# Optimization experiments

Hardware: AMD Instinct MI355X
Metric: run time of the kernel (lower is better)

Reference implementation:

```python
import jax, jax.numpy as jnp
import numpy as np

B, H, W, C = 2, 128, 128, 192
HEADS = 6
HD = C // HEADS
WS = 16
OWIN = int(WS * 0.5) + WS          # 24
PAD = (OWIN - WS) // 2             # 4
NQ = WS * WS
NK = OWIN * OWIN
EPS = 1e-6
HID = ((int(C * 2.667) + 7) // 8) * 8  # 512


def _rel_pos_index():
    cq = np.stack(np.meshgrid(np.arange(WS), np.arange(WS), indexing='ij')).reshape(2, -1)
    ck = np.stack(np.meshgrid(np.arange(OWIN), np.arange(OWIN), indexing='ij')).reshape(2, -1)
    rel = (ck[:, None, :] - cq[:, :, None]).transpose(1, 2, 0).astype(np.int64)  # (nq, nk, 2)
    rel[:, :, 0] += WS - 1
    rel[:, :, 1] += WS - 1
    rel[:, :, 0] *= WS + OWIN - 1
    return rel.sum(-1)  # (nq, nk)

RPI = jnp.asarray(_rel_pos_index())


def setup_inputs() -> dict:
    key = jax.random.key(0)
    ks = jax.random.split(key, 16)
    def w(k, shape, s=0.02):
        return jax.random.normal(k, shape, jnp.float32) * s
    return {
        'x': jax.random.normal(ks[0], (B, H * W, C), jnp.float32),
        'qkv_w': w(ks[1], (3 * C, C)), 'qkv_b': jnp.zeros((3 * C,), jnp.float32),
        'proj_w': w(ks[2], (C, C)), 'proj_b': jnp.zeros((C,), jnp.float32),
        'rpb': w(ks[3], ((WS + OWIN - 1) ** 2, HEADS)),
        'n1_w': jnp.ones((C,), jnp.float32), 'n1_b': jnp.zeros((C,), jnp.float32),
        'ls1': jnp.full((C,), 1e-6, jnp.float32),
        'n2_w': jnp.ones((C,), jnp.float32), 'n2_b': jnp.zeros((C,), jnp.float32),
        'ls2': jnp.full((C,), 1e-6, jnp.float32),
        'fcgv_w': w(ks[4], (2 * HID, C)), 'fcgv_b': jnp.zeros((2 * HID,), jnp.float32),
        'dw_w': w(ks[5], (HID, 1, 3, 3)), 'dw_b': jnp.zeros((HID,), jnp.float32),
        'dwd_w': w(ks[6], (HID, 1, 3, 3)), 'dwd_b': jnp.zeros((HID,), jnp.float32),
        'dil_scale': w(ks[7], (1,), 0.1),
        'fco_w': w(ks[8], (C, HID)), 'fco_b': jnp.zeros((C,), jnp.float32),
    }


def _iln(x, wgt, bias):
    # spatially-holistic LN: stats over (L, C); returns normed x and residual scale
    xf = x.astype(jnp.float32)
    mean = xf.mean(axis=(1, 2), keepdims=True)
    var = ((xf - mean) ** 2).mean(axis=(1, 2), keepdims=True)
    std = jnp.sqrt(var + EPS)
    scale = jnp.minimum(std, 2.0)  # std_ema buffer initialized to 1.0 (eval path)
    xn = (xf - mean) / scale
    return (xn * wgt + bias).astype(x.dtype), scale


def _oca(x, qkv_w, qkv_b, proj_w, proj_b, rpb):
    b = x.shape[0]
    nh, nw = H // WS, W // WS
    nwin = b * nh * nw
    qkv = x @ qkv_w.T + qkv_b
    q, k, v = jnp.split(qkv, 3, axis=-1)
    # non-overlapping query windows: (nwin, heads, nq, hd)
    qw = q.reshape(b, nh, WS, nw, WS, C).transpose(0, 1, 3, 2, 4, 5)
    qw = qw.reshape(nwin, NQ, HEADS, HD).transpose(0, 2, 1, 3)
    # overlapping K/V windows via unfold(kernel=OWIN, stride=WS, pad=PAD)
    kv = jnp.concatenate([k, v], axis=-1).reshape(b, H, W, 2 * C).transpose(0, 3, 1, 2)
    kvp = jnp.pad(kv, ((0, 0), (0, 0), (PAD, PAD), (PAD, PAD)))
    ih = (jnp.arange(nh) * WS)[:, None] + jnp.arange(OWIN)[None, :]
    iw = (jnp.arange(nw) * WS)[:, None] + jnp.arange(OWIN)[None, :]
    kvw = kvp[:, :, ih][:, :, :, :, iw]               # (b, 2C, nh, owin, nw, owin)
    kvw = kvw.transpose(0, 2, 4, 3, 5, 1).reshape(nwin, NK, 2 * C)
    kw = kvw[..., :C].reshape(nwin, NK, HEADS, HD).transpose(0, 2, 1, 3)
    vw = kvw[..., C:].reshape(nwin, NK, HEADS, HD).transpose(0, 2, 1, 3)
    bias = rpb[RPI].transpose(2, 0, 1)                # (heads, nq, nk)
    logits = jnp.einsum('whqd,whkd->whqk', qw, kw) * (HD ** -0.5) + bias
    attn = jax.nn.softmax(logits, axis=-1)
    out = jnp.einsum('whqk,whkd->whqd', attn, vw)
    out = out.transpose(0, 2, 1, 3).reshape(nwin, NQ, C) @ proj_w.T + proj_b
    # window reverse -> (b, H*W, C)
    out = out.reshape(b, nh, nw, WS, WS, C).transpose(0, 1, 3, 2, 4, 5).reshape(b, H * W, C)
    return out


def _dw(x, wgt, bias, dil):
    y = jax.lax.conv_general_dilated(x, wgt, (1, 1), [(dil, dil), (dil, dil)],
                                     rhs_dilation=(dil, dil), feature_group_count=HID)
    return y + bias[None, :, None, None]


def _ffn(x, fcgv_w, fcgv_b, dw_w, dw_b, dwd_w, dwd_b, dil_scale, fco_w, fco_b):
    gv = x @ fcgv_w.T + fcgv_b
    g, val = jnp.split(gv, 2, axis=-1)
    h = jax.nn.silu(g) * val
    h = h.transpose(0, 2, 1).reshape(-1, HID, H, W)
    h = _dw(h, dw_w, dw_b, 1)
    h = h + dil_scale[0] * _dw(h, dwd_w, dwd_b, 2)
    h = h.reshape(-1, HID, H * W).transpose(0, 2, 1)
    return h @ fco_w.T + fco_b


def reference(x, qkv_w, qkv_b, proj_w, proj_b, rpb, n1_w, n1_b, ls1, n2_w, n2_b, ls2,
              fcgv_w, fcgv_b, dw_w, dw_b, dwd_w, dwd_b, dil_scale, fco_w, fco_b):
    xn, std1 = _iln(x, n1_w, n1_b)
    x = x + std1 * (ls1 * _oca(xn, qkv_w, qkv_b, proj_w, proj_b, rpb))
    xn2, std2 = _iln(x, n2_w, n2_b)
    x = x + std2 * (ls2 * _ffn(xn2, fcgv_w, fcgv_b, dw_w, dw_b, dwd_w, dwd_b, dil_scale, fco_w, fco_b))
    return x
```

## Files before the change

kernel.cpp:

```cpp
#include <hip/hip_runtime.h>

#define DI __device__ __forceinline__

typedef __attribute__((ext_vector_type(8))) short bh8;
typedef __attribute__((ext_vector_type(4))) float fx4;
typedef __attribute__((ext_vector_type(16))) float fx16;

DI short f2bf(float f) {
  unsigned u = __builtin_bit_cast(unsigned, f);
  u += 0x7FFFu + ((u >> 16) & 1u);
  return (short)(u >> 16);
}
DI float bf2f(short s) {
  unsigned u = ((unsigned)(unsigned short)s) << 16;
  return __builtin_bit_cast(float, u);
}
DI fx4 mfma16(bh8 a, bh8 b, fx4 c) {
  return __builtin_amdgcn_mfma_f32_16x16x32_bf16(a, b, c, 0, 0, 0);
}
DI fx16 mfma32(bh8 a, bh8 b, fx16 c) {
  return __builtin_amdgcn_mfma_f32_32x32x16_bf16(a, b, c, 0, 0, 0);
}
DI fx4 fzero() { fx4 z = {0.f, 0.f, 0.f, 0.f}; return z; }

DI float fexp2(float x) {
#if __has_builtin(__builtin_amdgcn_exp2f)
  return __builtin_amdgcn_exp2f(x);
#else
  return exp2f(x);
#endif
}

DI bh8 pack8(const float* src) {
  fx4 v0 = *(const fx4*)src;
  fx4 v1 = *(const fx4*)(src + 4);
  bh8 pk;
#pragma unroll
  for (int j = 0; j < 4; j++) { pk[j] = f2bf(v0[j]); pk[j + 4] = f2bf(v1[j]); }
  return pk;
}

__global__ __launch_bounds__(256) void iln_partial(const float* __restrict__ x,
                                                   float* __restrict__ part) {
  const int blk = blockIdx.x, tid = threadIdx.x;
  const fx4* p = (const fx4*)(x + (size_t)blk * 12288);
  float s = 0.f, s2 = 0.f;
#pragma unroll
  for (int i = 0; i < 12; i++) {
    fx4 v = p[i * 256 + tid];
    s  += v[0] + v[1] + v[2] + v[3];
    s2 += v[0] * v[0] + v[1] * v[1] + v[2] * v[2] + v[3] * v[3];
  }
  __shared__ float sm[512];
  sm[tid] = s; sm[256 + tid] = s2;
  __syncthreads();
  for (int st = 128; st > 0; st >>= 1) {
    if (tid < st) { sm[tid] += sm[tid + st]; sm[256 + tid] += sm[256 + tid + st]; }
    __syncthreads();
  }
  if (tid == 0) { part[blk * 2] = sm[0]; part[blk * 2 + 1] = sm[256]; }
}

__global__ __launch_bounds__(256) void prep(const float* __restrict__ qkv_w,
                                            const float* __restrict__ proj_w,
                                            const float* __restrict__ fcgv_w,
                                            const float* __restrict__ fco_w,
                                            const float* __restrict__ rpb,
                                            short* __restrict__ wbuf,
                                            short* __restrict__ btb) {
  if (blockIdx.x < 216) {
    int t = blockIdx.x * 256 + threadIdx.x;
    int blk = t >> 6, lane = t & 63;
    int g = lane >> 4, h = lane & 15;
    const float* src;
    if (blk < 216) {
      int b2 = blk;
      int ni = b2 % 3; b2 /= 3;
      int wn = b2 & 1; b2 >>= 1;
      int kt = b2 % 6; b2 /= 6;
      int nt = b2;
      src = qkv_w + (size_t)(nt * 96 + wn * 48 + ni * 16 + h) * 192 + kt * 32 + g * 8;
    } else if (blk < 288) {
      int b2 = blk - 216;
      int ni = b2 % 3; b2 /= 3;
      int wn = b2 & 1; b2 >>= 1;
      int kt = b2 % 6; b2 /= 6;
      int nt = b2;
      src = proj_w + (size_t)(nt * 96 + wn * 48 + ni * 16 + h) * 192 + kt * 32 + g * 8;
    } else if (blk < 672) {
      int b2 = blk - 288;
      int gv = b2 & 1; b2 >>= 1;
      int ni = b2 & 1; b2 >>= 1;
      int wn = b2 & 1; b2 >>= 1;
      int kt = b2 % 6; b2 /= 6;
      int nt = b2;
      int r = wn * 32 + ni * 16 + h;
      int row = gv ? (512 + nt * 64 + r) : (nt * 64 + r);
      src = fcgv_w + (size_t)row * 192 + kt * 32 + g * 8;
    } else {
      int b2 = blk - 672;
      int ni = b2 % 3; b2 /= 3;
      int wn = b2 & 1; b2 >>= 1;
      int kt = b2 & 15; b2 >>= 4;
      int nt = b2;
      src = fco_w + (size_t)(nt * 96 + wn * 48 + ni * 16 + h) * 512 + kt * 32 + g * 8;
    }
    *(bh8*)(wbuf + (size_t)blk * 512 + lane * 8) = pack8(src);
  } else {
    int t = (blockIdx.x - 216) * 256 + threadIdx.x;
    int lane = t & 63;
    int u = t >> 6;
    int qi = u & 1;
    int c = lane & 31, hi = lane >> 5;
    int w = (u >> 2) / 9 % 4;
    int head = (u >> 2) / 36;
    int q = w * 64 + qi * 32 + c;
    int qterm = (q >> 4) * 39 + (q & 15);
    short o16[16];
#pragma unroll
    for (int r = 0; r < 16; r++) {
      int kk = ((u >> 2) % 9) * 64 + ((u >> 1) & 1) * 32 + (r & 3) + 8 * (r >> 2) + 4 * hi;
      int ky = (kk * 2731) >> 16;
      int kx = kk - ky * 24;
      int idx = ky * 39 + kx + 600 - qterm;
      o16[r] = f2bf(rpb[idx * 6 + head] * 1.4426950408889634f);
    }
    *(bh8*)(btb + (size_t)u * 1024 + lane * 16)     = *(bh8*)&o16[0];
    *(bh8*)(btb + (size_t)u * 1024 + lane * 16 + 8) = *(bh8*)&o16[8];
  }
}

__global__ __launch_bounds__(256) void cvt_aff(const float* __restrict__ src,
                                               const float* __restrict__ part,
                                               const float* __restrict__ w,
                                               const float* __restrict__ bias,
                                               short* __restrict__ dst,
                                               float* __restrict__ st) {
  __shared__ float rs[512];
  const int tid = threadIdx.x;
  const int bb = (blockIdx.x >= 1536) ? 1 : 0;
  rs[tid]       = part[(bb * 256 + tid) * 2];
  rs[256 + tid] = part[(bb * 256 + tid) * 2 + 1];
  __syncthreads();
  for (int s = 128; s > 0; s >>= 1) {
    if (tid < s) { rs[tid] += rs[tid + s]; rs[256 + tid] += rs[256 + tid + s]; }
    __syncthreads();
  }
  const float invn = 1.f / 3145728.f;
  float mean = rs[0] * invn;
  float var  = rs[256] * invn - mean * mean;
  float scale = fminf(sqrtf(var + 1e-6f), 2.f);
  if (tid == 0 && (blockIdx.x == 0 || blockIdx.x == 1536)) {
    st[bb * 2] = mean;
    st[bb * 2 + 1] = scale;
  }
  const float isc = 1.f / scale;
  int t = blockIdx.x * 256 + tid;
  int row = t / 24;
  int c0 = (t - row * 24) * 8;
  int mt = row >> 7, wm = (row >> 6) & 1, mi = (row >> 4) & 3, h = row & 15;
  int kt = c0 >> 5, g = (c0 >> 3) & 3;
  int blk = ((mt * 2 + wm) * 4 + mi) * 6 + kt;
  int lane = g * 16 + h;
  const float* sp = src + (size_t)row * 192 + c0;
  fx4 v0 = *(const fx4*)sp;
  fx4 v1 = *(const fx4*)(sp + 4);
  bh8 pk;
#pragma unroll
  for (int j = 0; j < 4; j++) {
    float a = w[c0 + j] * isc;
    pk[j] = f2bf(v0[j] * a + (bias[c0 + j] - mean * a));
  }
#pragma unroll
  for (int j = 0; j < 4; j++) {
    float a = w[c0 + 4 + j] * isc;
    pk[j + 4] = f2bf(v1[j] * a + (bias[c0 + 4 + j] - mean * a));
  }
  *(bh8*)(dst + (size_t)blk * 512 + lane * 8) = pk;
}

__global__ __launch_bounds__(256) void gemm_qkv(const short* __restrict__ xn,
                                                const short* __restrict__ wq,
                                                const float* __restrict__ wb,
                                                short* __restrict__ qb,
                                                short* __restrict__ kb,
                                                short* __restrict__ vb) {
  const int mt = blockIdx.x, by = blockIdx.y;
  const int m0 = mt * 128;
  const int tid = threadIdx.x, wid = tid >> 6, lane = tid & 63;
  const int g = lane >> 4, h = lane & 15;
  const int wm = wid >> 1, wn = wid & 1;
  fx4 acc[4][3];
#pragma unroll
  for (int i = 0; i < 4; i++)
#pragma unroll
    for (int j = 0; j < 3; j++) acc[i][j] = fzero();

#pragma unroll
  for (int kt = 0; kt < 6; kt++) {
    bh8 af[4], bf[3];
#pragma unroll
    for (int mi = 0; mi < 4; mi++)
      af[mi] = *(const bh8*)(xn + (size_t)((((mt * 2 + wm) * 4 + mi) * 6 + kt)) * 512 + lane * 8);
#pragma unroll
    for (int ni = 0; ni < 3; ni++)
      bf[ni] = *(const bh8*)(wq + (size_t)(((by * 6 + kt) * 2 + wn) * 3 + ni) * 512 + lane * 8);
#pragma unroll
    for (int ni = 0; ni < 3; ni++)
#pragma unroll
      for (int mi = 0; mi < 4; mi++) acc[mi][ni] = mfma16(af[mi], bf[ni], acc[mi][ni]);
  }
  const int seg = by >> 1;
  short* dst = (seg == 0) ? qb : (seg == 1 ? kb : vb);
  const float sc = (seg == 1) ? 0.25503486f : 1.0f;
  const int colbase = (by & 1) * 96;
#pragma unroll
  for (int mi = 0; mi < 4; mi++)
#pragma unroll
    for (int ni = 0; ni < 3; ni++)
#pragma unroll
      for (int r = 0; r < 4; r++) {
        int row = m0 + wm * 64 + mi * 16 + g * 4 + r;
        int col = colbase + wn * 48 + ni * 16 + h;
        dst[(size_t)row * 192 + col] = f2bf((acc[mi][ni][r] + wb[seg * 192 + col]) * sc);
      }
}

__global__ __launch_bounds__(256, 3) void attn_kernel(const short* __restrict__ qb,
                                                      const short* __restrict__ kb,
                                                      const short* __restrict__ vb,
                                                      const short* __restrict__ btb,
                                                      short* __restrict__ ao) {
  __shared__ short K_lds[64 * 40];
  __shared__ short Vt_lds[32 * 72];
  __shared__ float l_lds[256];
  const int tid = threadIdx.x;
  const int win = blockIdx.x, head = blockIdx.y;
  const int b = win >> 6, wy = (win >> 3) & 7, wx = win & 7;
  const int w = tid >> 6, lane = tid & 63, c = lane & 31, hi = lane >> 5;

  bh8 qf[2][2];
#pragma unroll
  for (int qi = 0; qi < 2; qi++) {
    int ql = w * 64 + qi * 32 + c;
    size_t gl = (size_t)(b * 16384 + (wy * 16 + (ql >> 4)) * 128 + wx * 16 + (ql & 15));
#pragma unroll
    for (int ds = 0; ds < 2; ds++)
      qf[qi][ds] = *(const bh8*)(qb + gl * 192 + head * 32 + ds * 16 + hi * 8);
  }
  float l_run[2] = {0.f, 0.f};
  fx16 out[2];
#pragma unroll
  for (int r = 0; r < 16; r++) { out[0][r] = 0.f; out[1][r] = 0.f; }

  const int hw9 = (head * 4 + w) * 9;

  const int kl_a = tid >> 2, part_a = tid & 3;
  const int kl_b = tid & 63, hg_b = tid >> 6;

  for (int kc = 0; kc < 9; kc++) {
    __syncthreads();
    {
      int key = kc * 64 + kl_a;
      int ky = key / 24, kx = key - ky * 24;
      int py = wy * 16 - 4 + ky, px = wx * 16 - 4 + kx;
      bh8 kv = {};
      if ((unsigned)py < 128u && (unsigned)px < 128u)
        kv = *(const bh8*)(kb + ((size_t)(b * 16384 + py * 128 + px)) * 192 + head * 32 + part_a * 8);
      *(bh8*)&K_lds[kl_a * 40 + part_a * 8] = kv;

      int key2 = kc * 64 + kl_b;
      int ky2 = key2 / 24, kx2 = key2 - ky2 * 24;
      int py2 = wy * 16 - 4 + ky2, px2 = wx * 16 - 4 + kx2;
      bh8 vv = {};
      if ((unsigned)py2 < 128u && (unsigned)px2 < 128u)
        vv = *(const bh8*)(vb + ((size_t)(b * 16384 + py2 * 128 + px2)) * 192 + head * 32 + hg_b * 8);
#pragma unroll
      for (int j = 0; j < 8; j++) Vt_lds[(hg_b * 8 + j) * 72 + kl_b] = vv[j];
    }
    __syncthreads();

    const short* base_kc = btb + (size_t)(hw9 + kc) * 4096 + lane * 16;
#pragma unroll
    for (int ki = 0; ki < 2; ki++) {
      fx16 st[2];
#pragma unroll
      for (int qi = 0; qi < 2; qi++) {
        const short* bp = base_kc + (ki * 2 + qi) * 1024;
        int4 b0 = *(const int4*)bp;
        int4 b1 = *(const int4*)(bp + 8);
#pragma unroll
        for (int d = 0; d < 4; d++) {
          unsigned u0 = ((const unsigned*)&b0)[d];
          unsigned u1 = ((const unsigned*)&b1)[d];
          st[qi][2 * d]     = __builtin_bit_cast(float, u0 << 16);
          st[qi][2 * d + 1] = __builtin_bit_cast(float, u0 & 0xffff0000u);
          st[qi][8 + 2 * d]     = __builtin_bit_cast(float, u1 << 16);
          st[qi][8 + 2 * d + 1] = __builtin_bit_cast(float, u1 & 0xffff0000u);
        }
      }
      __builtin_amdgcn_s_setprio(1);
#pragma unroll
      for (int ds = 0; ds < 2; ds++) {
        bh8 kf = *(bh8*)&K_lds[(ki * 32 + c) * 40 + ds * 16 + hi * 8];
        st[0] = mfma32(kf, qf[0][ds], st[0]);
        st[1] = mfma32(kf, qf[1][ds], st[1]);
      }
      __builtin_amdgcn_s_setprio(0);
#pragma unroll
      for (int qi = 0; qi < 2; qi++) {
        float s = 0.f;
#pragma unroll
        for (int r = 0; r < 16; r++) {
          float p = fexp2(st[qi][r]);
          st[qi][r] = p;
          s += p;
        }
        l_run[qi] += s;
      }
      int dwq[2][2][4];
#pragma unroll
      for (int qi = 0; qi < 2; qi++)
#pragma unroll
        for (int k1 = 0; k1 < 2; k1++)
#pragma unroll
          for (int p01 = 0; p01 < 2; p01++) {
            int rA = 2 * p01 + 8 * k1;
            int A, Bv;
            asm("v_cvt_pk_bf16_f32 %0, %1, %2" : "=v"(A)  : "v"(st[qi][rA]),     "v"(st[qi][rA + 1]));
            asm("v_cvt_pk_bf16_f32 %0, %1, %2" : "=v"(Bv) : "v"(st[qi][rA + 4]), "v"(st[qi][rA + 5]));
#if __has_builtin(__builtin_amdgcn_permlane32_swap)
            auto pr = __builtin_amdgcn_permlane32_swap((unsigned)A, (unsigned)Bv, false, false);
            dwq[qi][k1][p01]     = (int)pr[0];
            dwq[qi][k1][p01 + 2] = (int)pr[1];
#else
            int Ax = __shfl_xor(A, 32);
            int Bx = __shfl_xor(Bv, 32);
            dwq[qi][k1][p01]     = hi ? Bx : A;
            dwq[qi][k1][p01 + 2] = hi ? Bv : Ax;
#endif
          }
      __builtin_amdgcn_s_setprio(1);
#pragma unroll
      for (int k1 = 0; k1 < 2; k1++) {
        bh8 bv2 = *(bh8*)&Vt_lds[c * 72 + (ki * 2 + k1) * 16 + hi * 8];
#pragma unroll
        for (int qi = 0; qi < 2; qi++) {
          int4 t4 = {dwq[qi][k1][0], dwq[qi][k1][1], dwq[qi][k1][2], dwq[qi][k1][3]};
          out[qi] = mfma32(__builtin_bit_cast(bh8, t4), bv2, out[qi]);
        }
      }
      __builtin_amdgcn_s_setprio(0);
    }
  }
#pragma unroll
  for (int qi = 0; qi < 2; qi++) {
    float lp = l_run[qi] + __shfl_xor(l_run[qi], 32);
    l_lds[w * 64 + qi * 32 + c] = 1.f / lp;
  }
  __syncthreads();
#pragma unroll
  for (int qi = 0; qi < 2; qi++)
#pragma unroll
    for (int r = 0; r < 16; r++) {
      int row = (r & 3) + 8 * (r >> 2) + 4 * hi;
      float val = out[qi][r] * l_lds[w * 64 + qi * 32 + row];
      int ql = w * 64 + qi * 32 + row;
      ao[((size_t)(win * 256 + ql)) * 192 + head * 32 + c] = f2bf(val);
    }
}

__global__ __launch_bounds__(256) void gemm_proj(const short* __restrict__ ao,
                                                 const short* __restrict__ wp,
                                                 const float* __restrict__ wb,
                                                 const float* __restrict__ x,
                                                 const float* __restrict__ ls1,
                                                 const float* __restrict__ st,
                                                 float* __restrict__ x1,
                                                 float* __restrict__ part2) {
  __shared__ float red[512];
  const int m0 = blockIdx.x * 128, by = blockIdx.y;
  const int tid = threadIdx.x, wid = tid >> 6, lane = tid & 63;
  const int g = lane >> 4, h = lane & 15;
  const int wm = wid >> 1, wn = wid & 1;
  fx4 acc[4][3];
#pragma unroll
  for (int i = 0; i < 4; i++)
#pragma unroll
    for (int j = 0; j < 3; j++) acc[i][j] = fzero();

#pragma unroll
  for (int kt = 0; kt < 6; kt++) {
    bh8 af[4], bf[3];
#pragma unroll
    for (int mi = 0; mi < 4; mi++)
      af[mi] = *(const bh8*)(ao + (size_t)(m0 + wm * 64 + mi * 16 + h) * 192 + kt * 32 + g * 8);
#pragma unroll
    for (int ni = 0; ni < 3; ni++)
      bf[ni] = *(const bh8*)(wp + (size_t)(((by * 6 + kt) * 2 + wn) * 3 + ni) * 512 + lane * 8);
#pragma unroll
    for (int ni = 0; ni < 3; ni++)
#pragma unroll
      for (int mi = 0; mi < 4; mi++) acc[mi][ni] = mfma16(af[mi], bf[ni], acc[mi][ni]);
  }
  const int n0 = by * 96;
  float ps = 0.f, ps2 = 0.f;
#pragma unroll
  for (int mi = 0; mi < 4; mi++)
#pragma unroll
    for (int ni = 0; ni < 3; ni++)
#pragma unroll
      for (int r = 0; r < 4; r++) {
        int grow = m0 + wm * 64 + mi * 16 + g * 4 + r;
        int win = grow >> 8, q = grow & 255;
        int bb = win >> 6, wy = (win >> 3) & 7, wxx = win & 7;
        int l = (wy * 16 + (q >> 4)) * 128 + wxx * 16 + (q & 15);
        int col = n0 + wn * 48 + ni * 16 + h;
        size_t di = ((size_t)(bb * 16384 + l)) * 192 + col;
        float s1 = st[bb * 2 + 1];
        float val = x[di] + s1 * ls1[col] * (acc[mi][ni][r] + wb[col]);
        x1[di] = val;
        ps += val;
        ps2 += val * val;
      }
  red[tid] = ps; red[256 + tid] = ps2;
  __syncthreads();
  for (int s = 128; s > 0; s >>= 1) {
    if (tid < s) { red[tid] += red[tid + s]; red[256 + tid] += red[256 + tid + s]; }
    __syncthreads();
  }
  if (tid == 0) {
    int pi = blockIdx.x * 2 + by;
    part2[pi * 2] = red[0];
    part2[pi * 2 + 1] = red[256];
  }
}

__global__ __launch_bounds__(256) void gemm_fcgv(const short* __restrict__ x1n,
                                                 const short* __restrict__ wg,
                                                 const float* __restrict__ wb,
                                                 short* __restrict__ hp) {
  __shared__ short T[64 * 136];
  const int mt = blockIdx.x, by = blockIdx.y, n0 = by * 64;
  const int m0 = mt * 128;
  const int b = m0 >> 14, l0 = m0 & 16383;
  const int tid = threadIdx.x, wid = tid >> 6, lane = tid & 63;
  const int g = lane >> 4, h = lane & 15;
  const int wm = wid >> 1, wn = wid & 1;
  fx4 accg[4][2], accv[4][2];
#pragma unroll
  for (int i = 0; i < 4; i++)
#pragma unroll
    for (int j = 0; j < 2; j++) { accg[i][j] = fzero(); accv[i][j] = fzero(); }

#pragma unroll
  for (int kt = 0; kt < 6; kt++) {
    bh8 af[4], bg[2], bv[2];
#pragma unroll
    for (int mi = 0; mi < 4; mi++)
      af[mi] = *(const bh8*)(x1n + (size_t)((((mt * 2 + wm) * 4 + mi) * 6 + kt)) * 512 + lane * 8);
#pragma unroll
    for (int ni = 0; ni < 2; ni++) {
      size_t base = (size_t)((((by * 6 + kt) * 2 + wn) * 2 + ni) * 2) * 512;
      bg[ni] = *(const bh8*)(wg + base + lane * 8);
      bv[ni] = *(const bh8*)(wg + base + 512 + lane * 8);
    }
#pragma unroll
    for (int ni = 0; ni < 2; ni++)
#pragma unroll
      for (int mi = 0; mi < 4; mi++) {
        accg[mi][ni] = mfma16(af[mi], bg[ni], accg[mi][ni]);
        accv[mi][ni] = mfma16(af[mi], bv[ni], accv[mi][ni]);
      }
  }
  short hs[4][2][4];
#pragma unroll
  for (int mi = 0; mi < 4; mi++)
#pragma unroll
    for (int ni = 0; ni < 2; ni++)
#pragma unroll
      for (int r = 0; r < 4; r++) {
        int colg = n0 + wn * 32 + ni * 16 + h;
        float gv = accg[mi][ni][r] + wb[colg];
        float vv = accv[mi][ni][r] + wb[512 + colg];
        hs[mi][ni][r] = f2bf(gv / (1.f + __expf(-gv)) * vv);
      }
#pragma unroll
  for (int mi = 0; mi < 4; mi++)
#pragma unroll
    for (int ni = 0; ni < 2; ni++)
#pragma unroll
      for (int r = 0; r < 4; r++) {
        int cc = wn * 32 + ni * 16 + h;
        int rl = wm * 64 + mi * 16 + g * 4 + r;
        T[cc * 136 + rl] = hs[mi][ni][r];
      }
  __syncthreads();
#pragma unroll
  for (int i = 0; i < 4; i++) {
    int ch = tid + i * 256;
    int cc = ch >> 4, lg = ch & 15;
    bh8 v = *(bh8*)&T[cc * 136 + lg * 8];
    *(bh8*)(hp + (((size_t)(b * 512 + n0 + cc)) << 14) + l0 + lg * 8) = v;
  }
}

__global__ __launch_bounds__(256) void dw_fused(const short* __restrict__ in,
                                                const float* __restrict__ w1,
                                                const float* __restrict__ b1,
                                                const float* __restrict__ w2,
                                                const float* __restrict__ b2,
                                                const float* __restrict__ dsc,
                                                short* __restrict__ outp) {
  __shared__ short P[70 * 136];
  __shared__ short D[68 * 136];
  const int p = blockIdx.x >> 1, s = blockIdx.x & 1, c = p & 511;
  const int tid = threadIdx.x;
  const int r0 = s * 64;
  const int plo = s ? 61 : 0;
  const int pbase = r0 - 3;
  const int dlo = s ? 62 : 0;
  const int dbase = r0 - 2;
  const short* ip = in + ((size_t)p << 14);

  for (int i = tid; i < 67 * 16; i += 256) {
    int rr = plo + (i >> 4), sl = i & 15;
    bh8 v = *(const bh8*)(ip + rr * 128 + sl * 8);
    *(bh8*)&P[(rr - pbase) * 136 + sl * 8] = v;
  }
  float k1[9], k2[9];
#pragma unroll
  for (int j = 0; j < 9; j++) { k1[j] = w1[c * 9 + j]; k2[j] = w2[c * 9 + j]; }
  const float bias1 = b1[c], bias2 = b2[c], ds = dsc[0];
  __syncthreads();

  for (int i = tid; i < 66 * 16; i += 256) {
    int gy = dlo + (i >> 4);
    int x0 = (i & 15) * 8;
    float acc[8];
#pragma unroll
    for (int q = 0; q < 8; q++) acc[q] = bias1;
#pragma unroll
    for (int ky = 0; ky < 3; ky++) {
      int yy = gy + ky - 1;
      if ((unsigned)yy < 128u) {
        const short* row = &P[(yy - pbase) * 136];
        float f[10];
        bh8 v = *(const bh8*)&row[x0];
#pragma unroll
        for (int j = 0; j < 8; j++) f[j + 1] = bf2f(v[j]);
        f[0] = (x0 == 0) ? 0.f : bf2f(row[x0 - 1]);
        f[9] = (x0 == 120) ? 0.f : bf2f(row[x0 + 8]);
        float w0 = k1[ky * 3], wA = k1[ky * 3 + 1], wB = k1[ky * 3 + 2];
#pragma unroll
        for (int q = 0; q < 8; q++) acc[q] += f[q] * w0 + f[q + 1] * wA + f[q + 2] * wB;
      }
    }
    bh8 pk;
#pragma unroll
    for (int q = 0; q < 8; q++) pk[q] = f2bf(acc[q]);
    *(bh8*)&D[(gy - dbase) * 136 + x0] = pk;
  }
  __syncthreads();

  for (int i = tid; i < 64 * 16; i += 256) {
    int gy = r0 + (i >> 4);
    int x0 = (i & 15) * 8;
    float acc[8], center[8];
#pragma unroll
    for (int q = 0; q < 8; q++) acc[q] = bias2;
#pragma unroll
    for (int ky = 0; ky < 3; ky++) {
      int yy = gy + (ky - 1) * 2;
      if ((unsigned)yy < 128u) {
        const short* row = &D[(yy - dbase) * 136];
        float f[12];
        bh8 v = *(const bh8*)&row[x0];
#pragma unroll
        for (int j = 0; j < 8; j++) f[j + 2] = bf2f(v[j]);
        if (x0 == 0) { f[0] = 0.f; f[1] = 0.f; }
        else {
          unsigned lp = *(const unsigned*)&row[x0 - 2];
          f[0] = __builtin_bit_cast(float, lp << 16);
          f[1] = __builtin_bit_cast(float, lp & 0xffff0000u);
        }
        if (x0 == 120) { f[10] = 0.f; f[11] = 0.f; }
        else {
          unsigned rp = *(const unsigned*)&row[x0 + 8];
          f[10] = __builtin_bit_cast(float, rp << 16);
          f[11] = __builtin_bit_cast(float, rp & 0xffff0000u);
        }
        float w0 = k2[ky * 3], wA = k2[ky * 3 + 1], wB = k2[ky * 3 + 2];
#pragma unroll
        for (int q = 0; q < 8; q++) acc[q] += f[q] * w0 + f[q + 2] * wA + f[q + 4] * wB;
        if (ky == 1) {
#pragma unroll
          for (int q = 0; q < 8; q++) center[q] = f[q + 2];
        }
      }
    }
    bh8 pk;
#pragma unroll
    for (int q = 0; q < 8; q++) pk[q] = f2bf(center[q] + ds * acc[q]);
    *(bh8*)(outp + ((size_t)p << 14) + gy * 128 + x0) = pk;
  }
}

__global__ __launch_bounds__(256) void gemm_fco(const short* __restrict__ h2,
                                                const short* __restrict__ wo,
                                                const float* __restrict__ wb,
                                                const float* __restrict__ x1,
                                                const float* __restrict__ ls2,
                                                const float* __restrict__ st,
                                                float* __restrict__ out) {
  __shared__ short As[128 * 40];
  const int m0 = blockIdx.x * 128, by = blockIdx.y, n0 = by * 96;
  const int b = m0 >> 14, l0 = m0 & 16383;
  const int tid = threadIdx.x, wid = tid >> 6, lane = tid & 63;
  const int g = lane >> 4, h = lane & 15;
  const int wm = wid >> 1, wn = wid & 1;
  const int cp = tid & 15, lg = tid >> 4;
  fx4 acc[4][3];
#pragma unroll
  for (int i = 0; i < 4; i++)
#pragma unroll
    for (int j = 0; j < 3; j++) acc[i][j] = fzero();

  for (int kt = 0; kt < 16; kt++) {
    const int k0 = kt * 32;
    {
      const short* basep = h2 + (((size_t)(b * 512 + k0 + 2 * cp)) << 14) + l0 + lg * 8;
      bh8 v0 = *(const bh8*)basep;
      bh8 v1 = *(const bh8*)(basep + 16384);
#pragma unroll
      for (int j = 0; j < 8; j++) {
        unsigned pkv = (unsigned)(unsigned short)v0[j] | (((unsigned)(unsigned short)v1[j]) << 16);
        *(unsigned*)&As[(lg * 8 + j) * 40 + 2 * cp] = pkv;
      }
    }
    __syncthreads();
    bh8 af[4], bf[3];
#pragma unroll
    for (int mi = 0; mi < 4; mi++)
      af[mi] = *(bh8*)&As[(wm * 64 + mi * 16 + h) * 40 + g * 8];
#pragma unroll
    for (int ni = 0; ni < 3; ni++)
      bf[ni] = *(const bh8*)(wo + (size_t)(((by * 16 + kt) * 2 + wn) * 3 + ni) * 512 + lane * 8);
#pragma unroll
    for (int ni = 0; ni < 3; ni++)
#pragma unroll
      for (int mi = 0; mi < 4; mi++) acc[mi][ni] = mfma16(af[mi], bf[ni], acc[mi][ni]);
    __syncthreads();
  }
  float s2 = st[b * 2 + 1];
#pragma unroll
  for (int mi = 0; mi < 4; mi++)
#pragma unroll
    for (int ni = 0; ni < 3; ni++)
#pragma unroll
      for (int r = 0; r < 4; r++) {
        int row = m0 + wm * 64 + mi * 16 + g * 4 + r;
        int col = n0 + wn * 48 + ni * 16 + h;
        size_t di = (size_t)row * 192 + col;
        out[di] = x1[di] + s2 * ls2[col] * (acc[mi][ni][r] + wb[col]);
      }
}

extern "C" void kernel_launch(void* const* d_in, const int* in_sizes, int n_in,
                              void* d_out, int out_size, void* d_ws, size_t ws_size,
                              hipStream_t stream) {
  const float* x      = (const float*)d_in[0];
  const float* qkv_w  = (const float*)d_in[1];
  const float* qkv_b  = (const float*)d_in[2];
  const float* proj_w = (const float*)d_in[3];
  const float* proj_b = (const float*)d_in[4];
  const float* rpb    = (const float*)d_in[5];
  const float* n1_w   = (const float*)d_in[6];
  const float* n1_b   = (const float*)d_in[7];
  const float* ls1    = (const float*)d_in[8];
  const float* n2_w   = (const float*)d_in[9];
  const float* n2_b   = (const float*)d_in[10];
  const float* ls2    = (const float*)d_in[11];
  const float* fcgv_w = (const float*)d_in[12];
  const float* fcgv_b = (const float*)d_in[13];
  const float* dw_w   = (const float*)d_in[14];
  const float* dw_b   = (const float*)d_in[15];
  const float* dwd_w  = (const float*)d_in[16];
  const float* dwd_b  = (const float*)d_in[17];
  const float* dil    = (const float*)d_in[18];
  const float* fco_w  = (const float*)d_in[19];
  const float* fco_b  = (const float*)d_in[20];
  float* out = (float*)d_out;
  char* ws = (char*)d_ws;

  short* wbuf = (short*)(ws + 0);
  short* wq = wbuf;
  short* wp = wbuf + 110592;
  short* wg = wbuf + 147456;
  short* wo = wbuf + 344064;
  float* part  = (float*)(ws + 884736);
  float* st1   = (float*)(ws + 891904);
  float* st2   = (float*)(ws + 891968);
  float* part2 = (float*)(ws + 892032);
  short* xn  = (short*)(ws + 1048576);
  short* btb = (short*)(ws + 13631488);
  short* qb  = (short*)(ws + 17301504);
  short* kb  = (short*)(ws + 29884416);
  short* vb  = (short*)(ws + 42467328);
  short* ao  = (short*)(ws + 55050240);
  float* x1  = (float*)(ws + 1048576);
  short* x1n = (short*)(ws + 26214400);
  short* hp  = (short*)(ws + 42467328);
  short* h2  = (short*)(ws + 76021760);

  iln_partial<<<512, 256, 0, stream>>>(x, part);
  prep<<<432, 256, 0, stream>>>(qkv_w, proj_w, fcgv_w, fco_w, rpb, wbuf, btb);
  cvt_aff<<<3072, 256, 0, stream>>>(x, part, n1_w, n1_b, xn, st1);
  gemm_qkv<<<dim3(256, 6), 256, 0, stream>>>(xn, wq, qkv_b, qb, kb, vb);
  attn_kernel<<<dim3(128, 6), 256, 0, stream>>>(qb, kb, vb, btb, ao);
  gemm_proj<<<dim3(256, 2), 256, 0, stream>>>(ao, wp, proj_b, x, ls1, st1, x1, part2);
  cvt_aff<<<3072, 256, 0, stream>>>(x1, part2, n2_w, n2_b, x1n, st2);
  gemm_fcgv<<<dim3(256, 8), 256, 0, stream>>>(x1n, wg, fcgv_b, hp);
  dw_fused<<<2048, 256, 0, stream>>>(hp, dw_w, dw_b, dwd_w, dwd_b, dil, h2);
  gemm_fco<<<dim3(256, 2), 256, 0, stream>>>(h2, wo, fco_b, x1, ls2, st2, out);
}
```

Measured before the change: 173.6 us.

## Swap grid axes so N-tiles share A rows, double-buffer fco A tile

Swaps the grid dimensions of the QKV, attention, proj, fcgv and fco kernels so that blocks sharing the same row tile (or window) are launched next to each other, which should improve L2 reuse of activation data. In gemm_fco, the LDS A tile is double-buffered: the next k-tile's global load is issued before the MFMAs and written to the alternate buffer afterwards, which removes one barrier per iteration. Double buffering doubles that kernel's LDS use and adds register pressure from the prefetched values.

```diff
diff --git a/kernel.cpp b/kernel.cpp
--- a/kernel.cpp
+++ b/kernel.cpp
@@ -185,7 +185,7 @@
                                                 short* __restrict__ qb,
                                                 short* __restrict__ kb,
                                                 short* __restrict__ vb) {
-  const int mt = blockIdx.x, by = blockIdx.y;
+  const int by = blockIdx.x, mt = blockIdx.y;
   const int m0 = mt * 128;
   const int tid = threadIdx.x, wid = tid >> 6, lane = tid & 63;
   const int g = lane >> 4, h = lane & 15;
@@ -235,7 +235,7 @@
   __shared__ short Vt_lds[32 * 72];
   __shared__ float l_lds[256];
   const int tid = threadIdx.x;
-  const int win = blockIdx.x, head = blockIdx.y;
+  const int win = blockIdx.y, head = blockIdx.x;
   const int b = win >> 6, wy = (win >> 3) & 7, wx = win & 7;
   const int w = tid >> 6, lane = tid & 63, c = lane & 31, hi = lane >> 5;
 
@@ -379,7 +379,8 @@
                                                  float* __restrict__ x1,
                                                  float* __restrict__ part2) {
   __shared__ float red[512];
-  const int m0 = blockIdx.x * 128, by = blockIdx.y;
+  const int by = blockIdx.x, mt = blockIdx.y;
+  const int m0 = mt * 128;
   const int tid = threadIdx.x, wid = tid >> 6, lane = tid & 63;
   const int g = lane >> 4, h = lane & 15;
   const int wm = wid >> 1, wn = wid & 1;
@@ -430,7 +431,7 @@
     __syncthreads();
   }
   if (tid == 0) {
-    int pi = blockIdx.x * 2 + by;
+    int pi = mt * 2 + by;
     part2[pi * 2] = red[0];
     part2[pi * 2 + 1] = red[256];
   }
@@ -441,7 +442,7 @@
                                                  const float* __restrict__ wb,
                                                  short* __restrict__ hp) {
   __shared__ short T[64 * 136];
-  const int mt = blockIdx.x, by = blockIdx.y, n0 = by * 64;
+  const int by = blockIdx.x, mt = blockIdx.y, n0 = by * 64;
   const int m0 = mt * 128;
   const int b = m0 >> 14, l0 = m0 & 16383;
   const int tid = threadIdx.x, wid = tid >> 6, lane = tid & 63;
@@ -613,8 +614,9 @@
                                                 const float* __restrict__ ls2,
                                                 const float* __restrict__ st,
                                                 float* __restrict__ out) {
-  __shared__ short As[128 * 40];
-  const int m0 = blockIdx.x * 128, by = blockIdx.y, n0 = by * 96;
+  __shared__ short As[2][128 * 40];
+  const int by = blockIdx.x, mt = blockIdx.y, n0 = by * 96;
+  const int m0 = mt * 128;
   const int b = m0 >> 14, l0 = m0 & 16383;
   const int tid = threadIdx.x, wid = tid >> 6, lane = tid & 63;
   const int g = lane >> 4, h = lane & 15;
@@ -626,23 +628,32 @@
 #pragma unroll
     for (int j = 0; j < 3; j++) acc[i][j] = fzero();
 
+  auto loadA = [&](int kt, bh8& v0, bh8& v1) {
+    const short* basep = h2 + (((size_t)(b * 512 + kt * 32 + 2 * cp)) << 14) + l0 + lg * 8;
+    v0 = *(const bh8*)basep;
+    v1 = *(const bh8*)(basep + 16384);
+  };
+  auto writeA = [&](int buf, bh8 v0, bh8 v1) {
+#pragma unroll
+    for (int j = 0; j < 8; j++) {
+      unsigned pkv = (unsigned)(unsigned short)v0[j] | (((unsigned)(unsigned short)v1[j]) << 16);
+      *(unsigned*)&As[buf][(lg * 8 + j) * 40 + 2 * cp] = pkv;
+    }
+  };
+  {
+    bh8 c0, c1;
+    loadA(0, c0, c1);
+    writeA(0, c0, c1);
+  }
+  int cur = 0;
   for (int kt = 0; kt < 16; kt++) {
-    const int k0 = kt * 32;
-    {
-      const short* basep = h2 + (((size_t)(b * 512 + k0 + 2 * cp)) << 14) + l0 + lg * 8;
-      bh8 v0 = *(const bh8*)basep;
-      bh8 v1 = *(const bh8*)(basep + 16384);
-#pragma unroll
-      for (int j = 0; j < 8; j++) {
-        unsigned pkv = (unsigned)(unsigned short)v0[j] | (((unsigned)(unsigned short)v1[j]) << 16);
-        *(unsigned*)&As[(lg * 8 + j) * 40 + 2 * cp] = pkv;
-      }
-    }
     __syncthreads();
+    bh8 n0v, n1v;
+    if (kt < 15) loadA(kt + 1, n0v, n1v);
     bh8 af[4], bf[3];
 #pragma unroll
     for (int mi = 0; mi < 4; mi++)
-      af[mi] = *(bh8*)&As[(wm * 64 + mi * 16 + h) * 40 + g * 8];
+      af[mi] = *(bh8*)&As[cur][(wm * 64 + mi * 16 + h) * 40 + g * 8];
 #pragma unroll
     for (int ni = 0; ni < 3; ni++)
       bf[ni] = *(const bh8*)(wo + (size_t)(((by * 16 + kt) * 2 + wn) * 3 + ni) * 512 + lane * 8);
@@ -650,7 +661,8 @@
     for (int ni = 0; ni < 3; ni++)
 #pragma unroll
       for (int mi = 0; mi < 4; mi++) acc[mi][ni] = mfma16(af[mi], bf[ni], acc[mi][ni]);
-    __syncthreads();
+    if (kt < 15) writeA(cur ^ 1, n0v, n1v);
+    cur ^= 1;
   }
   float s2 = st[b * 2 + 1];
 #pragma unroll
@@ -716,11 +728,11 @@
   iln_partial<<<512, 256, 0, stream>>>(x, part);
   prep<<<432, 256, 0, stream>>>(qkv_w, proj_w, fcgv_w, fco_w, rpb, wbuf, btb);
   cvt_aff<<<3072, 256, 0, stream>>>(x, part, n1_w, n1_b, xn, st1);
-  gemm_qkv<<<dim3(256, 6), 256, 0, stream>>>(xn, wq, qkv_b, qb, kb, vb);
-  attn_kernel<<<dim3(128, 6), 256, 0, stream>>>(qb, kb, vb, btb, ao);
-  gemm_proj<<<dim3(256, 2), 256, 0, stream>>>(ao, wp, proj_b, x, ls1, st1, x1, part2);
+  gemm_qkv<<<dim3(6, 256), 256, 0, stream>>>(xn, wq, qkv_b, qb, kb, vb);
+  attn_kernel<<<dim3(6, 128), 256, 0, stream>>>(qb, kb, vb, btb, ao);
+  gemm_proj<<<dim3(2, 256), 256, 0, stream>>>(ao, wp, proj_b, x, ls1, st1, x1, part2);
   cvt_aff<<<3072, 256, 0, stream>>>(x1, part2, n2_w, n2_b, x1n, st2);
-  gemm_fcgv<<<dim3(256, 8), 256, 0, stream>>>(x1n, wg, fcgv_b, hp);
+  gemm_fcgv<<<dim3(8, 256), 256, 0, stream>>>(x1n, wg, fcgv_b, hp);
   dw_fused<<<2048, 256, 0, stream>>>(hp, dw_w, dw_b, dwd_w, dwd_b, dil, h2);
-  gemm_fco<<<dim3(256, 2), 256, 0, stream>>>(h2, wo, fco_b, x1, ls2, st2, out);
-}
+  gemm_fco<<<dim3(2, 256), 256, 0, stream>>>(h2, wo, fco_b, x1, ls2, st2, out);
+}
```

New measurement: 183.8 us. 1.06x slower.
